# Optimization experiments

Measured on AMD Instinct MI355X. Metric: run time of the kernel, lower is better.

Reference implementation:

```python
import jax, jax.numpy as jnp
import numpy as np

N = 40000
E = 640000
IN = 1300
H = 4
C = 64
G = 64  # number of graphs in the batch
NEG_SLOPE = 0.2


def gat_conv(x, edge_index, W, att_src, att_dst, bias):
    """PyG-style GATConv with default add_self_loops=True, concat heads.
    x: [N, F_in], W: [F_in, H*C], att_src/att_dst: [H, C], bias: [H*C].
    edge_index[0]=source j, edge_index[1]=target i (messages flow j->i).
    """
    n = x.shape[0]
    h = (x @ W).reshape(n, H, C)                      # [N, H, C]
    loop = jnp.arange(n, dtype=edge_index.dtype)
    src = jnp.concatenate([edge_index[0], loop])      # [E+N]
    dst = jnp.concatenate([edge_index[1], loop])      # [E+N]
    a_src = jnp.einsum('nhc,hc->nh', h, att_src)      # [N, H]
    a_dst = jnp.einsum('nhc,hc->nh', h, att_dst)      # [N, H]
    e = jax.nn.leaky_relu(a_src[src] + a_dst[dst], NEG_SLOPE)  # [E+N, H]
    # segment softmax over incoming edges of each target node
    e_max = jax.ops.segment_max(e, dst, num_segments=n)
    e = jnp.exp(e - e_max[dst])
    denom = jax.ops.segment_sum(e, dst, num_segments=n)
    alpha = e / (denom[dst] + 1e-16)                  # [E+N, H]
    msg = h[src] * alpha[:, :, None]                  # [E+N, H, C]
    out = jax.ops.segment_sum(msg, dst, num_segments=n)  # [N, H, C]
    return out.reshape(n, H * C) + bias


def global_mean_pool(x, batch, num_graphs):
    s = jax.ops.segment_sum(x, batch, num_segments=num_graphs)
    cnt = jax.ops.segment_sum(jnp.ones((x.shape[0],), x.dtype), batch,
                              num_segments=num_graphs)
    return s / jnp.maximum(cnt, 1.0)[:, None]


def setup_inputs() -> dict:
    key = jax.random.key(0)
    ks = jax.random.split(key, 12)
    x = jax.random.normal(ks[0], (N, IN), dtype=jnp.float32)
    edge_index = jax.random.randint(ks[1], (2, E), 0, N, dtype=jnp.int64)
    batch = jnp.sort(jax.random.randint(ks[2], (N,), 0, G, dtype=jnp.int64))
    s1 = 1.0 / np.sqrt(IN)
    s2 = 1.0 / np.sqrt(H * C)
    W1 = jax.random.normal(ks[3], (IN, H * C), dtype=jnp.float32) * s1
    att_src1 = jax.random.normal(ks[4], (H, C), dtype=jnp.float32) * s2
    att_dst1 = jax.random.normal(ks[5], (H, C), dtype=jnp.float32) * s2
    b1 = jnp.zeros((H * C,), jnp.float32)
    W2 = jax.random.normal(ks[6], (H * C, H * C), dtype=jnp.float32) * s2
    att_src2 = jax.random.normal(ks[7], (H, C), dtype=jnp.float32) * s2
    att_dst2 = jax.random.normal(ks[8], (H, C), dtype=jnp.float32) * s2
    b2 = jnp.zeros((H * C,), jnp.float32)
    lin_w = jax.random.normal(ks[9], (H * C, 1), dtype=jnp.float32) * s2
    lin_b = jnp.zeros((1,), jnp.float32)
    return {"x": x, "edge_index": edge_index, "batch": batch,
            "W1": W1, "att_src1": att_src1, "att_dst1": att_dst1, "b1": b1,
            "W2": W2, "att_src2": att_src2, "att_dst2": att_dst2, "b2": b2,
            "lin_w": lin_w, "lin_b": lin_b}


def reference(x, edge_index, batch, W1, att_src1, att_dst1, b1,
              W2, att_src2, att_dst2, b2, lin_w, lin_b):
    h = jax.nn.relu(gat_conv(x, edge_index, W1, att_src1, att_dst1, b1))
    h = jax.nn.relu(gat_conv(h, edge_index, W2, att_src2, att_dst2, b2))
    p = global_mean_pool(h, batch, G)                 # [G, H*C]
    out = p @ lin_w + lin_b                           # [G, 1]
    return out.squeeze()                              # [G]
```

## Files before the change

kernel.cpp:

```cpp
#include <hip/hip_runtime.h>
#include <hip/hip_bf16.h>

#define N_NODES 40000
#define N_EDGES 640000
#define F_IN    1300
#define NH      4
#define NC      64
#define F_OUT   256
#define NG      64
#define NEG_SLOPE 0.2f

typedef short short8v __attribute__((ext_vector_type(8)));
typedef float f32x16  __attribute__((ext_vector_type(16)));

__device__ __forceinline__ float lrelu(float x) { return x >= 0.f ? x : NEG_SLOPE * x; }

__device__ __forceinline__ short f2bf(float v) {
    unsigned u = __builtin_bit_cast(unsigned, v);
    unsigned r = (u + 0x7fffu + ((u >> 16) & 1u)) >> 16;
    return (short)r;
}
__device__ __forceinline__ float bf2f(short s) {
    unsigned u = ((unsigned)(unsigned short)s) << 16;
    return __builtin_bit_cast(float, u);
}

__device__ __forceinline__ short8v ld8(const short* p) {
    short4 a = *(const short4*)(p);
    short4 b = *(const short4*)(p + 4);
    short8v r;
    r[0] = a.x; r[1] = a.y; r[2] = a.z; r[3] = a.w;
    r[4] = b.x; r[5] = b.y; r[6] = b.z; r[7] = b.w;
    return r;
}
__device__ __forceinline__ void st8(short* p, short8v v) {
    short4 a, b;
    a.x = v[0]; a.y = v[1]; a.z = v[2]; a.w = v[3];
    b.x = v[4]; b.y = v[5]; b.z = v[6]; b.w = v[7];
    *(short4*)(p)     = a;
    *(short4*)(p + 4) = b;
}

__device__ __forceinline__ void cvt8(const float4 a, const float4 b,
                                     short8v &h, short8v &l)
{
    h[0] = f2bf(a.x); l[0] = f2bf(a.x - bf2f(h[0]));
    h[1] = f2bf(a.y); l[1] = f2bf(a.y - bf2f(h[1]));
    h[2] = f2bf(a.z); l[2] = f2bf(a.z - bf2f(h[2]));
    h[3] = f2bf(a.w); l[3] = f2bf(a.w - bf2f(h[3]));
    h[4] = f2bf(b.x); l[4] = f2bf(b.x - bf2f(h[4]));
    h[5] = f2bf(b.y); l[5] = f2bf(b.y - bf2f(h[5]));
    h[6] = f2bf(b.z); l[6] = f2bf(b.z - bf2f(h[6]));
    h[7] = f2bf(b.w); l[7] = f2bf(b.w - bf2f(h[7]));
}

__global__ void wsplit_kernel(const float* __restrict__ W, short* __restrict__ hi,
                              short* __restrict__ lo, int K, int Kp)
{
    int idx = blockIdx.x * 256 + threadIdx.x;
    if (idx >= F_OUT * Kp) return;
    int n = idx / Kp, k = idx - n * Kp;
    float v = (k < K) ? W[(size_t)k * F_OUT + n] : 0.f;
    short h = f2bf(v);
    short l = f2bf(v - bf2f(h));
    hi[idx] = h;
    lo[idx] = l;
}

#define LDB 36

__global__ __launch_bounds__(256, 2) void gemm_mfma_kernel(
    const float* __restrict__ A, const short* __restrict__ Bth,
    const short* __restrict__ Btl, float* __restrict__ C, int K, int Kp)
{
    __shared__ short Bs_hi[2][256][LDB];
    __shared__ short Bs_lo[2][256][LDB];

    const int t     = threadIdx.x;
    const int lane  = t & 63;
    const int wv    = t >> 6;
    const int mr    = lane & 31;
    const int khalf = (lane >> 5) * 8;
    const int rbase = blockIdx.x * 64 + (wv >> 1) * 32;
    const int cbase = (wv & 1) * 128;

    f32x16 acc[4];
#pragma unroll
    for (int j = 0; j < 4; ++j)
#pragma unroll
        for (int r = 0; r < 16; ++r) acc[j][r] = 0.f;

    const int nt = Kp / 32;
    const size_t arow = (size_t)(rbase + mr) * K;
    const size_t bcol = (size_t)t * Kp;

    auto loadA8 = [&](int kg, float4 &x, float4 &y) {
        if (kg + 8 <= K) {
            x = *(const float4*)&A[arow + kg];
            y = *(const float4*)&A[arow + kg + 4];
        } else {
            float v0 = (kg + 0 < K) ? A[arow + kg + 0] : 0.f;
            float v1 = (kg + 1 < K) ? A[arow + kg + 1] : 0.f;
            float v2 = (kg + 2 < K) ? A[arow + kg + 2] : 0.f;
            float v3 = (kg + 3 < K) ? A[arow + kg + 3] : 0.f;
            float v4 = (kg + 4 < K) ? A[arow + kg + 4] : 0.f;
            float v5 = (kg + 5 < K) ? A[arow + kg + 5] : 0.f;
            float v6 = (kg + 6 < K) ? A[arow + kg + 6] : 0.f;
            float v7 = (kg + 7 < K) ? A[arow + kg + 7] : 0.f;
            x = make_float4(v0, v1, v2, v3);
            y = make_float4(v4, v5, v6, v7);
        }
    };

    short8v pbh0, pbh1, pbh2, pbh3, pbl0, pbl1, pbl2, pbl3;
    pbh0 = *(const short8v*)&Bth[bcol + 0];
    pbh1 = *(const short8v*)&Bth[bcol + 8];
    pbh2 = *(const short8v*)&Bth[bcol + 16];
    pbh3 = *(const short8v*)&Bth[bcol + 24];
    pbl0 = *(const short8v*)&Btl[bcol + 0];
    pbl1 = *(const short8v*)&Btl[bcol + 8];
    pbl2 = *(const short8v*)&Btl[bcol + 16];
    pbl3 = *(const short8v*)&Btl[bcol + 24];
    float4 a0x, a0y, a1x, a1y;
    loadA8(khalf, a0x, a0y);
    loadA8(16 + khalf, a1x, a1y);
    st8(&Bs_hi[0][t][0],  pbh0);
    st8(&Bs_hi[0][t][8],  pbh1);
    st8(&Bs_hi[0][t][16], pbh2);
    st8(&Bs_hi[0][t][24], pbh3);
    st8(&Bs_lo[0][t][0],  pbl0);
    st8(&Bs_lo[0][t][8],  pbl1);
    st8(&Bs_lo[0][t][16], pbl2);
    st8(&Bs_lo[0][t][24], pbl3);
    asm volatile("s_waitcnt lgkmcnt(0)" ::: "memory");
    __builtin_amdgcn_sched_barrier(0);
    __builtin_amdgcn_s_barrier();

    for (int it = 0; it < nt; ++it) {
        const int buf  = it & 1;
        const bool more = (it + 1 < nt);
        const int k0n  = (it + 1) * 32;

        short8v nbh0, nbh1, nbh2, nbh3, nbl0, nbl1, nbl2, nbl3;
        float4 na0x, na0y, na1x, na1y;
        if (more) {
            nbh0 = *(const short8v*)&Bth[bcol + k0n + 0];
            nbh1 = *(const short8v*)&Bth[bcol + k0n + 8];
            nbh2 = *(const short8v*)&Bth[bcol + k0n + 16];
            nbh3 = *(const short8v*)&Bth[bcol + k0n + 24];
            nbl0 = *(const short8v*)&Btl[bcol + k0n + 0];
            nbl1 = *(const short8v*)&Btl[bcol + k0n + 8];
            nbl2 = *(const short8v*)&Btl[bcol + k0n + 16];
            nbl3 = *(const short8v*)&Btl[bcol + k0n + 24];
            loadA8(k0n + khalf, na0x, na0y);
            loadA8(k0n + 16 + khalf, na1x, na1y);
        } else {
            nbh0 = nbh1 = nbh2 = nbh3 = (short8v)0;
            nbl0 = nbl1 = nbl2 = nbl3 = (short8v)0;
            na0x = na0y = na1x = na1y = make_float4(0.f, 0.f, 0.f, 0.f);
        }

        {
            short8v ah, al;
            cvt8(a0x, a0y, ah, al);
#pragma unroll
            for (int cf = 0; cf < 4; ++cf) {
                const short* ph = &Bs_hi[buf][cbase + cf * 32 + mr][khalf];
                const short* pl = &Bs_lo[buf][cbase + cf * 32 + mr][khalf];
                short8v bh = ld8(ph);
                short8v bl = ld8(pl);
                acc[cf] = __builtin_amdgcn_mfma_f32_32x32x16_bf16(ah, bh, acc[cf], 0, 0, 0);
                acc[cf] = __builtin_amdgcn_mfma_f32_32x32x16_bf16(ah, bl, acc[cf], 0, 0, 0);
                acc[cf] = __builtin_amdgcn_mfma_f32_32x32x16_bf16(al, bh, acc[cf], 0, 0, 0);
            }
            cvt8(a1x, a1y, ah, al);
#pragma unroll
            for (int cf = 0; cf < 4; ++cf) {
                const short* ph = &Bs_hi[buf][cbase + cf * 32 + mr][16 + khalf];
                const short* pl = &Bs_lo[buf][cbase + cf * 32 + mr][16 + khalf];
                short8v bh = ld8(ph);
                short8v bl = ld8(pl);
                acc[cf] = __builtin_amdgcn_mfma_f32_32x32x16_bf16(ah, bh, acc[cf], 0, 0, 0);
                acc[cf] = __builtin_amdgcn_mfma_f32_32x32x16_bf16(ah, bl, acc[cf], 0, 0, 0);
                acc[cf] = __builtin_amdgcn_mfma_f32_32x32x16_bf16(al, bh, acc[cf], 0, 0, 0);
            }
        }

        if (more) {
            st8(&Bs_hi[buf ^ 1][t][0],  nbh0);
            st8(&Bs_hi[buf ^ 1][t][8],  nbh1);
            st8(&Bs_hi[buf ^ 1][t][16], nbh2);
            st8(&Bs_hi[buf ^ 1][t][24], nbh3);
            st8(&Bs_lo[buf ^ 1][t][0],  nbl0);
            st8(&Bs_lo[buf ^ 1][t][8],  nbl1);
            st8(&Bs_lo[buf ^ 1][t][16], nbl2);
            st8(&Bs_lo[buf ^ 1][t][24], nbl3);
        }
        asm volatile("s_waitcnt lgkmcnt(0)" ::: "memory");
        __builtin_amdgcn_sched_barrier(0);
        __builtin_amdgcn_s_barrier();

        a0x = na0x; a0y = na0y; a1x = na1x; a1y = na1y;
    }

#pragma unroll
    for (int cf = 0; cf < 4; ++cf)
#pragma unroll
        for (int r = 0; r < 16; ++r) {
            int row = rbase + (r & 3) + 8 * (r >> 2) + 4 * (lane >> 5);
            int col = cbase + cf * 32 + mr;
            C[(size_t)row * F_OUT + col] = acc[cf][r];
        }
}

__global__ __launch_bounds__(256) void attn_coef_kernel(const float* __restrict__ h,
                                                        const float* __restrict__ att_s,
                                                        const float* __restrict__ att_d,
                                                        float* __restrict__ a_s,
                                                        float* __restrict__ a_d)
{
    const int n = blockIdx.x;
    const int t = threadIdx.x;
    const int w = t >> 6;
    const int l = t & 63;
    float hv = h[(size_t)n * F_OUT + t];
    float vs = hv * att_s[t];
    float vd = hv * att_d[t];
#pragma unroll
    for (int o = 1; o < 64; o <<= 1) {
        vs += __shfl_xor(vs, o);
        vd += __shfl_xor(vd, o);
    }
    if (l == 0) {
        a_s[n * NH + w] = vs;
        a_d[n * NH + w] = vd;
    }
}

__global__ void hist_kernel(const int* __restrict__ ei, int* __restrict__ deg)
{
    int e = blockIdx.x * blockDim.x + threadIdx.x;
    if (e < N_EDGES) atomicAdd(&deg[ei[N_EDGES + e]], 1);
}

__global__ __launch_bounds__(1024) void scan_kernel(const int* __restrict__ deg,
                                                    int* __restrict__ rowptr)
{
    __shared__ int sums[1024];
    const int t = threadIdx.x;
    const int chunk = (N_NODES + 1023) / 1024;
    int beg = t * chunk;
    int end = beg + chunk; if (end > N_NODES) end = N_NODES;
    if (beg > N_NODES) beg = N_NODES;
    int s = 0;
    for (int i = beg; i < end; ++i) s += deg[i];
    sums[t] = s;
    __syncthreads();
    for (int o = 1; o < 1024; o <<= 1) {
        int v = (t >= o) ? sums[t - o] : 0;
        __syncthreads();
        sums[t] += v;
        __syncthreads();
    }
    int run = (t == 0) ? 0 : sums[t - 1];
    for (int i = beg; i < end; ++i) { rowptr[i] = run; run += deg[i]; }
    if (t == 1023) rowptr[N_NODES] = run;
}

__global__ void scatter_kernel(const int* __restrict__ ei, int* __restrict__ cursor,
                               int* __restrict__ ssrc, int* __restrict__ edst)
{
    int e = blockIdx.x * blockDim.x + threadIdx.x;
    if (e < N_EDGES) {
        int d = ei[N_EDGES + e];
        int pos = atomicAdd(&cursor[d], 1);
        ssrc[pos] = ei[e];
        edst[pos] = d;
    }
}

__global__ void edge_logit_kernel(const int* __restrict__ ssrc,
                                  const int* __restrict__ edst,
                                  const float* __restrict__ a_s,
                                  const float* __restrict__ a_d,
                                  float* __restrict__ e_csr)
{
    int p = blockIdx.x * 256 + threadIdx.x;
    if (p >= N_EDGES) return;
    int s = ssrc[p], d = edst[p];
    float4 as = ((const float4*)a_s)[s];
    float4 ad = ((const float4*)a_d)[d];
    float4 e;
    e.x = lrelu(as.x + ad.x);
    e.y = lrelu(as.y + ad.y);
    e.z = lrelu(as.z + ad.z);
    e.w = lrelu(as.w + ad.w);
    ((float4*)e_csr)[p] = e;
}

__global__ __launch_bounds__(256) void agg_kernel(const float* __restrict__ h,
                                                  const float* __restrict__ e_csr,
                                                  const float* __restrict__ a_s,
                                                  const float* __restrict__ a_d,
                                                  const int* __restrict__ rowptr,
                                                  const int* __restrict__ ssrc,
                                                  const float* __restrict__ bias,
                                                  float* __restrict__ out)
{
    const int wv = threadIdx.x >> 6;
    const int n  = blockIdx.x * 4 + wv;
    const int l  = threadIdx.x & 63;

    const int beg = rowptr[n];
    const int deg = rowptr[n + 1] - beg;

    const int hA = l & 3;
    const float es = lrelu(a_s[n * NH + hA] + a_d[n * NH + hA]);
    const float* ep = e_csr + (size_t)beg * 4;

    float mx = es;
    for (int base = 0; base < deg; base += 16) {
        int i = base + (l >> 2);
        float e = (i < deg) ? ep[(size_t)i * 4 + hA] : -1e30f;
        mx = fmaxf(mx, e);
    }
#pragma unroll
    for (int o = 4; o < 64; o <<= 1) mx = fmaxf(mx, __shfl_xor(mx, o));

    float sm = ((l >> 2) == 0) ? __expf(es - mx) : 0.f;
    for (int base = 0; base < deg; base += 16) {
        int i = base + (l >> 2);
        sm += (i < deg) ? __expf(ep[(size_t)i * 4 + hA] - mx) : 0.f;
    }
#pragma unroll
    for (int o = 4; o < 64; o <<= 1) sm += __shfl_xor(sm, o);
    const float dinv = 1.f / (sm + 1e-16f);

    const int hB = l >> 4;
    const float mxB = __shfl(mx, hB);
    const float dvB = __shfl(dinv, hB);
    const float esB = __shfl(es, hB);

    const float4* h4 = (const float4*)h;
    float4 acc;
    {
        float sa = __expf(esB - mxB) * dvB;
        float4 hv = h4[(size_t)n * 64 + l];
        acc.x = sa * hv.x; acc.y = sa * hv.y; acc.z = sa * hv.z; acc.w = sa * hv.w;
    }
    int i = 0;
    for (; i + 8 <= deg; i += 8) {
        const int p = beg + i;
        int   s[8]; float e[8]; float4 v[8];
#pragma unroll
        for (int j = 0; j < 8; ++j) s[j] = ssrc[p + j];
#pragma unroll
        for (int j = 0; j < 8; ++j) e[j] = e_csr[(size_t)(p + j) * 4 + hB];
#pragma unroll
        for (int j = 0; j < 8; ++j) v[j] = h4[(size_t)s[j] * 64 + l];
#pragma unroll
        for (int j = 0; j < 8; ++j) {
            float a = __expf(e[j] - mxB) * dvB;
            acc.x += a * v[j].x; acc.y += a * v[j].y;
            acc.z += a * v[j].z; acc.w += a * v[j].w;
        }
    }
    for (; i < deg; ++i) {
        const int p = beg + i;
        int sj = ssrc[p];
        float a = __expf(e_csr[(size_t)p * 4 + hB] - mxB) * dvB;
        float4 hv = h4[(size_t)sj * 64 + l];
        acc.x += a * hv.x; acc.y += a * hv.y; acc.z += a * hv.z; acc.w += a * hv.w;
    }
    float4 bv = ((const float4*)bias)[l];
    float4 ov;
    ov.x = fmaxf(acc.x + bv.x, 0.f);
    ov.y = fmaxf(acc.y + bv.y, 0.f);
    ov.z = fmaxf(acc.z + bv.z, 0.f);
    ov.w = fmaxf(acc.w + bv.w, 0.f);
    ((float4*)out)[(size_t)n * 64 + l] = ov;
}

__global__ void ghist_kernel(const int* __restrict__ batch, int* __restrict__ gcnt)
{
    int n = blockIdx.x * blockDim.x + threadIdx.x;
    if (n < N_NODES) atomicAdd(&gcnt[batch[n]], 1);
}

__global__ __launch_bounds__(256) void pool_kernel(const float* __restrict__ x,
                                                   const int* __restrict__ gcnt,
                                                   const float* __restrict__ lin_w,
                                                   const float* __restrict__ lin_b,
                                                   float* __restrict__ out)
{
    const int g = blockIdx.x;
    const int t = threadIdx.x;
    __shared__ int s_start;
    if (t == 0) {
        int s = 0;
        for (int i = 0; i < g; ++i) s += gcnt[i];
        s_start = s;
    }
    __syncthreads();
    const int start = s_start;
    const int cnt = gcnt[g];
    float acc = 0.f;
    for (int i = 0; i < cnt; ++i) acc += x[(size_t)(start + i) * F_OUT + t];
    float p = acc / fmaxf((float)cnt, 1.f);
    float v = p * lin_w[t];
    __shared__ float red[256];
    red[t] = v;
    __syncthreads();
    for (int o = 128; o > 0; o >>= 1) {
        if (t < o) red[t] += red[t + o];
        __syncthreads();
    }
    if (t == 0) out[g] = red[0] + lin_b[0];
}

extern "C" void kernel_launch(void* const* d_in, const int* in_sizes, int n_in,
                              void* d_out, int out_size, void* d_ws, size_t ws_size,
                              hipStream_t stream)
{
    const float* x      = (const float*)d_in[0];
    const int*   ei     = (const int*)  d_in[1];
    const int*   batch  = (const int*)  d_in[2];
    const float* W1     = (const float*)d_in[3];
    const float* att_s1 = (const float*)d_in[4];
    const float* att_d1 = (const float*)d_in[5];
    const float* b1     = (const float*)d_in[6];
    const float* W2     = (const float*)d_in[7];
    const float* att_s2 = (const float*)d_in[8];
    const float* att_d2 = (const float*)d_in[9];
    const float* b2     = (const float*)d_in[10];
    const float* lin_w  = (const float*)d_in[11];
    const float* lin_b  = (const float*)d_in[12];
    float* out = (float*)d_out;

    const int Kp1 = 1312;
    const int Kp2 = 256;

    size_t off = 0;
    auto carve = [&](size_t bytes) -> void* {
        void* p = (char*)d_ws + off;
        off += (bytes + 255) & ~(size_t)255;
        return p;
    };
    float* hA     = (float*)carve((size_t)N_NODES * F_OUT * 4);
    float* hB     = (float*)carve((size_t)N_NODES * F_OUT * 4);
    float* a_s    = (float*)carve((size_t)N_NODES * NH * 4);
    float* a_d    = (float*)carve((size_t)N_NODES * NH * 4);
    int*   deg    = (int*)  carve((size_t)(N_NODES + 1) * 4);
    int*   rowptr = (int*)  carve((size_t)(N_NODES + 1) * 4);
    int*   cursor = (int*)  carve((size_t)N_NODES * 4);
    int*   ssrc   = (int*)  carve((size_t)N_EDGES * 4);
    int*   edst   = (int*)  carve((size_t)N_EDGES * 4);
    float* e_csr  = (float*)carve((size_t)N_EDGES * NH * 4);
    int*   gcnt   = (int*)  carve((size_t)NG * 4);
    short* Bt1h   = (short*)carve((size_t)F_OUT * Kp1 * 2);
    short* Bt1l   = (short*)carve((size_t)F_OUT * Kp1 * 2);
    short* Bt2h   = (short*)carve((size_t)F_OUT * Kp2 * 2);
    short* Bt2l   = (short*)carve((size_t)F_OUT * Kp2 * 2);
    (void)ws_size; (void)n_in; (void)in_sizes; (void)out_size;

    hipMemsetAsync(deg, 0, (size_t)(N_NODES + 1) * 4, stream);
    hipMemsetAsync(gcnt, 0, (size_t)NG * 4, stream);
    hist_kernel<<<(N_EDGES + 255) / 256, 256, 0, stream>>>(ei, deg);
    scan_kernel<<<1, 1024, 0, stream>>>(deg, rowptr);
    hipMemcpyAsync(cursor, rowptr, (size_t)N_NODES * 4, hipMemcpyDeviceToDevice, stream);
    scatter_kernel<<<(N_EDGES + 255) / 256, 256, 0, stream>>>(ei, cursor, ssrc, edst);
    ghist_kernel<<<(N_NODES + 255) / 256, 256, 0, stream>>>(batch, gcnt);
    wsplit_kernel<<<(F_OUT * Kp1 + 255) / 256, 256, 0, stream>>>(W1, Bt1h, Bt1l, F_IN, Kp1);
    wsplit_kernel<<<(F_OUT * Kp2 + 255) / 256, 256, 0, stream>>>(W2, Bt2h, Bt2l, F_OUT, Kp2);

    const int gblocks = N_NODES / 64;
    const int ablocks = N_NODES / 4;
    const int eblocks = (N_EDGES + 255) / 256;

    gemm_mfma_kernel<<<gblocks, 256, 0, stream>>>(x, Bt1h, Bt1l, hA, F_IN, Kp1);
    attn_coef_kernel<<<N_NODES, 256, 0, stream>>>(hA, att_s1, att_d1, a_s, a_d);
    edge_logit_kernel<<<eblocks, 256, 0, stream>>>(ssrc, edst, a_s, a_d, e_csr);
    agg_kernel<<<ablocks, 256, 0, stream>>>(hA, e_csr, a_s, a_d, rowptr, ssrc, b1, hB);

    gemm_mfma_kernel<<<gblocks, 256, 0, stream>>>(hB, Bt2h, Bt2l, hA, F_OUT, Kp2);
    attn_coef_kernel<<<N_NODES, 256, 0, stream>>>(hA, att_s2, att_d2, a_s, a_d);
    edge_logit_kernel<<<eblocks, 256, 0, stream>>>(ssrc, edst, a_s, a_d, e_csr);
    agg_kernel<<<ablocks, 256, 0, stream>>>(hA, e_csr, a_s, a_d, rowptr, ssrc, b2, hB);

    pool_kernel<<<NG, 256, 0, stream>>>(hB, gcnt, lin_w, lin_b, out);
}
```

Before: 1.208 ms.

## Stream B fragments directly from packed global layout; vectorize attn coef and split pooling

The GEMM drops the LDS double-buffer and barriers. It repacks the split-bf16 weights into a k/8-major layout so each lane loads its MFMA B fragment straight from global/L2. Each block now computes 32 rows with each wave covering 64 columns, which raises occupancy but makes B reuse depend on cache. Separately, the attention-coefficient kernel handles four nodes per block with float4 loads, and pooling is split four ways per graph and combined with atomicAdd after zeroing the output.

New measurement: 1.071 ms. -11.4%, faster.

```diff
diff --git a/kernel.cpp b/kernel.cpp
--- a/kernel.cpp
+++ b/kernel.cpp
@@ -25,22 +25,6 @@
     return __builtin_bit_cast(float, u);
 }
 
-__device__ __forceinline__ short8v ld8(const short* p) {
-    short4 a = *(const short4*)(p);
-    short4 b = *(const short4*)(p + 4);
-    short8v r;
-    r[0] = a.x; r[1] = a.y; r[2] = a.z; r[3] = a.w;
-    r[4] = b.x; r[5] = b.y; r[6] = b.z; r[7] = b.w;
-    return r;
-}
-__device__ __forceinline__ void st8(short* p, short8v v) {
-    short4 a, b;
-    a.x = v[0]; a.y = v[1]; a.z = v[2]; a.w = v[3];
-    b.x = v[4]; b.y = v[5]; b.z = v[6]; b.w = v[7];
-    *(short4*)(p)     = a;
-    *(short4*)(p + 4) = b;
-}
-
 __device__ __forceinline__ void cvt8(const float4 a, const float4 b,
                                      short8v &h, short8v &l)
 {
@@ -63,36 +47,40 @@
     float v = (k < K) ? W[(size_t)k * F_OUT + n] : 0.f;
     short h = f2bf(v);
     short l = f2bf(v - bf2f(h));
-    hi[idx] = h;
-    lo[idx] = l;
-}
-
-#define LDB 36
-
-__global__ __launch_bounds__(256, 2) void gemm_mfma_kernel(
-    const float* __restrict__ A, const short* __restrict__ Bth,
-    const short* __restrict__ Btl, float* __restrict__ C, int K, int Kp)
-{
-    __shared__ short Bs_hi[2][256][LDB];
-    __shared__ short Bs_lo[2][256][LDB];
-
+    size_t po = ((size_t)(k >> 3) * F_OUT + n) * 8 + (k & 7);
+    hi[po] = h;
+    lo[po] = l;
+}
+
+#define BMR 32
+
+__global__ __launch_bounds__(256, 3) void gemm_mfma_kernel(
+    const float* __restrict__ A, const short* __restrict__ Bph,
+    const short* __restrict__ Bpl, float* __restrict__ C, int K, int Kp)
+{
     const int t     = threadIdx.x;
     const int lane  = t & 63;
     const int wv    = t >> 6;
     const int mr    = lane & 31;
-    const int khalf = (lane >> 5) * 8;
-    const int rbase = blockIdx.x * 64 + (wv >> 1) * 32;
-    const int cbase = (wv & 1) * 128;
-
-    f32x16 acc[4];
-#pragma unroll
-    for (int j = 0; j < 4; ++j)
+    const int hs    = lane >> 5;
+    const int khalf = hs * 8;
+    const int rbase = blockIdx.x * BMR;
+    const int cbase = wv * 64;
+
+    f32x16 acc[2];
+#pragma unroll
+    for (int j = 0; j < 2; ++j)
 #pragma unroll
         for (int r = 0; r < 16; ++r) acc[j][r] = 0.f;
 
     const int nt = Kp / 32;
     const size_t arow = (size_t)(rbase + mr) * K;
-    const size_t bcol = (size_t)t * Kp;
+    const int col0 = cbase + mr;
+    const int col1 = cbase + 32 + mr;
+
+    auto bptr = [&](const short* Bp, int kk, int col) -> const short8v* {
+        return (const short8v*)&Bp[((size_t)(kk >> 3) * F_OUT + col) * 8];
+    };
 
     auto loadA8 = [&](int kg, float4 &x, float4 &y) {
         if (kg + 8 <= K) {
@@ -112,102 +100,70 @@
         }
     };
 
-    short8v pbh0, pbh1, pbh2, pbh3, pbl0, pbl1, pbl2, pbl3;
-    pbh0 = *(const short8v*)&Bth[bcol + 0];
-    pbh1 = *(const short8v*)&Bth[bcol + 8];
-    pbh2 = *(const short8v*)&Bth[bcol + 16];
-    pbh3 = *(const short8v*)&Bth[bcol + 24];
-    pbl0 = *(const short8v*)&Btl[bcol + 0];
-    pbl1 = *(const short8v*)&Btl[bcol + 8];
-    pbl2 = *(const short8v*)&Btl[bcol + 16];
-    pbl3 = *(const short8v*)&Btl[bcol + 24];
     float4 a0x, a0y, a1x, a1y;
+    short8v bh00, bh10, bh01, bh11, bl00, bl10, bl01, bl11;
     loadA8(khalf, a0x, a0y);
     loadA8(16 + khalf, a1x, a1y);
-    st8(&Bs_hi[0][t][0],  pbh0);
-    st8(&Bs_hi[0][t][8],  pbh1);
-    st8(&Bs_hi[0][t][16], pbh2);
-    st8(&Bs_hi[0][t][24], pbh3);
-    st8(&Bs_lo[0][t][0],  pbl0);
-    st8(&Bs_lo[0][t][8],  pbl1);
-    st8(&Bs_lo[0][t][16], pbl2);
-    st8(&Bs_lo[0][t][24], pbl3);
-    asm volatile("s_waitcnt lgkmcnt(0)" ::: "memory");
-    __builtin_amdgcn_sched_barrier(0);
-    __builtin_amdgcn_s_barrier();
+    bh00 = *bptr(Bph, khalf,      col0);
+    bh10 = *bptr(Bph, khalf,      col1);
+    bh01 = *bptr(Bph, 16 + khalf, col0);
+    bh11 = *bptr(Bph, 16 + khalf, col1);
+    bl00 = *bptr(Bpl, khalf,      col0);
+    bl10 = *bptr(Bpl, khalf,      col1);
+    bl01 = *bptr(Bpl, 16 + khalf, col0);
+    bl11 = *bptr(Bpl, 16 + khalf, col1);
 
     for (int it = 0; it < nt; ++it) {
-        const int buf  = it & 1;
         const bool more = (it + 1 < nt);
-        const int k0n  = (it + 1) * 32;
-
-        short8v nbh0, nbh1, nbh2, nbh3, nbl0, nbl1, nbl2, nbl3;
+        const int k0n = (it + 1) * 32;
+
         float4 na0x, na0y, na1x, na1y;
+        short8v nh00, nh10, nh01, nh11, nl00, nl10, nl01, nl11;
         if (more) {
-            nbh0 = *(const short8v*)&Bth[bcol + k0n + 0];
-            nbh1 = *(const short8v*)&Bth[bcol + k0n + 8];
-            nbh2 = *(const short8v*)&Bth[bcol + k0n + 16];
-            nbh3 = *(const short8v*)&Bth[bcol + k0n + 24];
-            nbl0 = *(const short8v*)&Btl[bcol + k0n + 0];
-            nbl1 = *(const short8v*)&Btl[bcol + k0n + 8];
-            nbl2 = *(const short8v*)&Btl[bcol + k0n + 16];
-            nbl3 = *(const short8v*)&Btl[bcol + k0n + 24];
             loadA8(k0n + khalf, na0x, na0y);
             loadA8(k0n + 16 + khalf, na1x, na1y);
+            nh00 = *bptr(Bph, k0n + khalf,      col0);
+            nh10 = *bptr(Bph, k0n + khalf,      col1);
+            nh01 = *bptr(Bph, k0n + 16 + khalf, col0);
+            nh11 = *bptr(Bph, k0n + 16 + khalf, col1);
+            nl00 = *bptr(Bpl, k0n + khalf,      col0);
+            nl10 = *bptr(Bpl, k0n + khalf,      col1);
+            nl01 = *bptr(Bpl, k0n + 16 + khalf, col0);
+            nl11 = *bptr(Bpl, k0n + 16 + khalf, col1);
         } else {
-            nbh0 = nbh1 = nbh2 = nbh3 = (short8v)0;
-            nbl0 = nbl1 = nbl2 = nbl3 = (short8v)0;
             na0x = na0y = na1x = na1y = make_float4(0.f, 0.f, 0.f, 0.f);
+            nh00 = nh10 = nh01 = nh11 = (short8v)0;
+            nl00 = nl10 = nl01 = nl11 = (short8v)0;
         }
 
         {
             short8v ah, al;
             cvt8(a0x, a0y, ah, al);
-#pragma unroll
-            for (int cf = 0; cf < 4; ++cf) {
-                const short* ph = &Bs_hi[buf][cbase + cf * 32 + mr][khalf];
-                const short* pl = &Bs_lo[buf][cbase + cf * 32 + mr][khalf];
-                short8v bh = ld8(ph);
-                short8v bl = ld8(pl);
-                acc[cf] = __builtin_amdgcn_mfma_f32_32x32x16_bf16(ah, bh, acc[cf], 0, 0, 0);
-                acc[cf] = __builtin_amdgcn_mfma_f32_32x32x16_bf16(ah, bl, acc[cf], 0, 0, 0);
-                acc[cf] = __builtin_amdgcn_mfma_f32_32x32x16_bf16(al, bh, acc[cf], 0, 0, 0);
-            }
+            acc[0] = __builtin_amdgcn_mfma_f32_32x32x16_bf16(ah, bh00, acc[0], 0, 0, 0);
+            acc[0] = __builtin_amdgcn_mfma_f32_32x32x16_bf16(ah, bl00, acc[0], 0, 0, 0);
+            acc[0] = __builtin_amdgcn_mfma_f32_32x32x16_bf16(al, bh00, acc[0], 0, 0, 0);
+            acc[1] = __builtin_amdgcn_mfma_f32_32x32x16_bf16(ah, bh10, acc[1], 0, 0, 0);
+            acc[1] = __builtin_amdgcn_mfma_f32_32x32x16_bf16(ah, bl10, acc[1], 0, 0, 0);
+            acc[1] = __builtin_amdgcn_mfma_f32_32x32x16_bf16(al, bh10, acc[1], 0, 0, 0);
             cvt8(a1x, a1y, ah, al);
-#pragma unroll
-            for (int cf = 0; cf < 4; ++cf) {
-                const short* ph = &Bs_hi[buf][cbase + cf * 32 + mr][16 + khalf];
-                const short* pl = &Bs_lo[buf][cbase + cf * 32 + mr][16 + khalf];
-                short8v bh = ld8(ph);
-                short8v bl = ld8(pl);
-                acc[cf] = __builtin_amdgcn_mfma_f32_32x32x16_bf16(ah, bh, acc[cf], 0, 0, 0);
-                acc[cf] = __builtin_amdgcn_mfma_f32_32x32x16_bf16(ah, bl, acc[cf], 0, 0, 0);
-                acc[cf] = __builtin_amdgcn_mfma_f32_32x32x16_bf16(al, bh, acc[cf], 0, 0, 0);
-            }
+            acc[0] = __builtin_amdgcn_mfma_f32_32x32x16_bf16(ah, bh01, acc[0], 0, 0, 0);
+            acc[0] = __builtin_amdgcn_mfma_f32_32x32x16_bf16(ah, bl01, acc[0], 0, 0, 0);
+            acc[0] = __builtin_amdgcn_mfma_f32_32x32x16_bf16(al, bh01, acc[0], 0, 0, 0);
+            acc[1] = __builtin_amdgcn_mfma_f32_32x32x16_bf16(ah, bh11, acc[1], 0, 0, 0);
+            acc[1] = __builtin_amdgcn_mfma_f32_32x32x16_bf16(ah, bl11, acc[1], 0, 0, 0);
+            acc[1] = __builtin_amdgcn_mfma_f32_32x32x16_bf16(al, bh11, acc[1], 0, 0, 0);
         }
 
-        if (more) {
-            st8(&Bs_hi[buf ^ 1][t][0],  nbh0);
-            st8(&Bs_hi[buf ^ 1][t][8],  nbh1);
-            st8(&Bs_hi[buf ^ 1][t][16], nbh2);
-            st8(&Bs_hi[buf ^ 1][t][24], nbh3);
-            st8(&Bs_lo[buf ^ 1][t][0],  nbl0);
-            st8(&Bs_lo[buf ^ 1][t][8],  nbl1);
-            st8(&Bs_lo[buf ^ 1][t][16], nbl2);
-            st8(&Bs_lo[buf ^ 1][t][24], nbl3);
-        }
-        asm volatile("s_waitcnt lgkmcnt(0)" ::: "memory");
-        __builtin_amdgcn_sched_barrier(0);
-        __builtin_amdgcn_s_barrier();
-
         a0x = na0x; a0y = na0y; a1x = na1x; a1y = na1y;
-    }
-
-#pragma unroll
-    for (int cf = 0; cf < 4; ++cf)
+        bh00 = nh00; bh10 = nh10; bh01 = nh01; bh11 = nh11;
+        bl00 = nl00; bl10 = nl10; bl01 = nl01; bl11 = nl11;
+    }
+
+#pragma unroll
+    for (int cf = 0; cf < 2; ++cf)
 #pragma unroll
         for (int r = 0; r < 16; ++r) {
-            int row = rbase + (r & 3) + 8 * (r >> 2) + 4 * (lane >> 5);
+            int row = rbase + (r & 3) + 8 * (r >> 2) + 4 * hs;
             int col = cbase + cf * 32 + mr;
             C[(size_t)row * F_OUT + col] = acc[cf][r];
         }
@@ -219,21 +175,22 @@
                                                         float* __restrict__ a_s,
                                                         float* __restrict__ a_d)
 {
-    const int n = blockIdx.x;
-    const int t = threadIdx.x;
-    const int w = t >> 6;
-    const int l = t & 63;
-    float hv = h[(size_t)n * F_OUT + t];
-    float vs = hv * att_s[t];
-    float vd = hv * att_d[t];
-#pragma unroll
-    for (int o = 1; o < 64; o <<= 1) {
+    const int wv = threadIdx.x >> 6;
+    const int n  = blockIdx.x * 4 + wv;
+    const int l  = threadIdx.x & 63;
+    float4 hv = ((const float4*)h)[(size_t)n * 64 + l];
+    float4 as = ((const float4*)att_s)[l];
+    float4 ad = ((const float4*)att_d)[l];
+    float vs = hv.x * as.x + hv.y * as.y + hv.z * as.z + hv.w * as.w;
+    float vd = hv.x * ad.x + hv.y * ad.y + hv.z * ad.z + hv.w * ad.w;
+#pragma unroll
+    for (int o = 1; o < 16; o <<= 1) {
         vs += __shfl_xor(vs, o);
         vd += __shfl_xor(vd, o);
     }
-    if (l == 0) {
-        a_s[n * NH + w] = vs;
-        a_d[n * NH + w] = vd;
+    if ((l & 15) == 0) {
+        a_s[n * NH + (l >> 4)] = vs;
+        a_d[n * NH + (l >> 4)] = vd;
     }
 }
 
@@ -393,7 +350,8 @@
                                                    const float* __restrict__ lin_b,
                                                    float* __restrict__ out)
 {
-    const int g = blockIdx.x;
+    const int g = blockIdx.x >> 2;
+    const int q = blockIdx.x & 3;
     const int t = threadIdx.x;
     __shared__ int s_start;
     if (t == 0) {
@@ -404,10 +362,13 @@
     __syncthreads();
     const int start = s_start;
     const int cnt = gcnt[g];
+    const int chunk = (cnt + 3) >> 2;
+    int i0 = q * chunk;
+    int i1 = i0 + chunk; if (i1 > cnt) i1 = cnt;
+    if (i0 > cnt) i0 = cnt;
     float acc = 0.f;
-    for (int i = 0; i < cnt; ++i) acc += x[(size_t)(start + i) * F_OUT + t];
-    float p = acc / fmaxf((float)cnt, 1.f);
-    float v = p * lin_w[t];
+    for (int i = i0; i < i1; ++i) acc += x[(size_t)(start + i) * F_OUT + t];
+    float v = acc / fmaxf((float)cnt, 1.f) * lin_w[t];
     __shared__ float red[256];
     red[t] = v;
     __syncthreads();
@@ -415,7 +376,7 @@
         if (t < o) red[t] += red[t + o];
         __syncthreads();
     }
-    if (t == 0) out[g] = red[0] + lin_b[0];
+    if (t == 0) atomicAdd(&out[g], red[0] + (q == 0 ? lin_b[0] : 0.f));
 }
 
 extern "C" void kernel_launch(void* const* d_in, const int* in_sizes, int n_in,
@@ -465,6 +426,7 @@
 
     hipMemsetAsync(deg, 0, (size_t)(N_NODES + 1) * 4, stream);
     hipMemsetAsync(gcnt, 0, (size_t)NG * 4, stream);
+    hipMemsetAsync(out, 0, (size_t)NG * 4, stream);
     hist_kernel<<<(N_EDGES + 255) / 256, 256, 0, stream>>>(ei, deg);
     scan_kernel<<<1, 1024, 0, stream>>>(deg, rowptr);
     hipMemcpyAsync(cursor, rowptr, (size_t)N_NODES * 4, hipMemcpyDeviceToDevice, stream);
@@ -473,19 +435,19 @@
     wsplit_kernel<<<(F_OUT * Kp1 + 255) / 256, 256, 0, stream>>>(W1, Bt1h, Bt1l, F_IN, Kp1);
     wsplit_kernel<<<(F_OUT * Kp2 + 255) / 256, 256, 0, stream>>>(W2, Bt2h, Bt2l, F_OUT, Kp2);
 
-    const int gblocks = N_NODES / 64;
+    const int gblocks = N_NODES / BMR;
     const int ablocks = N_NODES / 4;
     const int eblocks = (N_EDGES + 255) / 256;
 
     gemm_mfma_kernel<<<gblocks, 256, 0, stream>>>(x, Bt1h, Bt1l, hA, F_IN, Kp1);
-    attn_coef_kernel<<<N_NODES, 256, 0, stream>>>(hA, att_s1, att_d1, a_s, a_d);
+    attn_coef_kernel<<<ablocks, 256, 0, stream>>>(hA, att_s1, att_d1, a_s, a_d);
     edge_logit_kernel<<<eblocks, 256, 0, stream>>>(ssrc, edst, a_s, a_d, e_csr);
     agg_kernel<<<ablocks, 256, 0, stream>>>(hA, e_csr, a_s, a_d, rowptr, ssrc, b1, hB);
 
     gemm_mfma_kernel<<<gblocks, 256, 0, stream>>>(hB, Bt2h, Bt2l, hA, F_OUT, Kp2);
-    attn_coef_kernel<<<N_NODES, 256, 0, stream>>>(hA, att_s2, att_d2, a_s, a_d);
+    attn_coef_kernel<<<ablocks, 256, 0, stream>>>(hA, att_s2, att_d2, a_s, a_d);
     edge_logit_kernel<<<eblocks, 256, 0, stream>>>(ssrc, edst, a_s, a_d, e_csr);
     agg_kernel<<<ablocks, 256, 0, stream>>>(hA, e_csr, a_s, a_d, rowptr, ssrc, b2, hB);
 
-    pool_kernel<<<NG, 256, 0, stream>>>(hB, gcnt, lin_w, lin_b, out);
-}
+    pool_kernel<<<NG * 4, 256, 0, stream>>>(hB, gcnt, lin_w, lin_b, out);
+}
```
